# Performance work log

Measured on AMD Instinct MI355X. Metric: run time of the kernel, lower is better.

## Reference

```python
import jax, jax.numpy as jnp
import numpy as np

KEEP_RATIO = 0.1
FS = 8          # feature_size
BN_EPS = 1e-5


def dct_matrix(N):
    # Orthonormal DCT-II matrix: D[k,n] = s_k * cos(pi*(2n+1)*k/(2N))
    n = jnp.arange(N, dtype=jnp.float32)
    k = n[:, None]
    D = jnp.cos(jnp.pi * (2.0 * n + 1.0) * k / (2.0 * N))
    scale = jnp.full((N, 1), jnp.sqrt(2.0 / N), jnp.float32).at[0, 0].set(jnp.sqrt(1.0 / N))
    return D * scale


def bilinear_resize(x, out_h, out_w):
    # torch F.interpolate bilinear, align_corners=False (half-pixel centers, no antialias)
    def coords(in_size, out):
        src = (jnp.arange(out, dtype=jnp.float32) + 0.5) * (in_size / out) - 0.5
        src = jnp.clip(src, 0.0, in_size - 1.0)
        i0 = jnp.floor(src).astype(jnp.int32)
        i1 = jnp.minimum(i0 + 1, in_size - 1)
        return i0, i1, src - i0.astype(jnp.float32)
    r0, r1, rw = coords(x.shape[2], out_h)
    c0, c1, cw = coords(x.shape[3], out_w)
    x = x[:, :, r0, :] * (1.0 - rw)[:, None] + x[:, :, r1, :] * rw[:, None]
    x = x[:, :, :, c0] * (1.0 - cw) + x[:, :, :, c1] * cw
    return x


def apply_dct(x):
    H, W = x.shape[2], x.shape[3]
    Dh, Dw = dct_matrix(H), dct_matrix(W)
    # 2D DCT-II (ortho): Y = Dh @ X @ Dw^T
    y = jnp.einsum('hi,bcij,wj->bchw', Dh, x, Dw)
    hk, wk = int(H * KEEP_RATIO), int(W * KEEP_RATIO)
    mask = jnp.zeros((H, W), x.dtype).at[:hk, :wk].set(1.0)  # low-pass keep top-left block
    y = y * mask
    # inverse DCT (ortho): X = Dh^T @ Y @ Dw
    x = jnp.einsum('ih,bchw,jw->bcij', Dh, y, Dw)
    return bilinear_resize(x, FS, FS)


def generate_gradient_image(x):
    # scipy convolve2d flips the kernel, but flipped sobel == -sobel and we take abs,
    # so plain correlation with sobel is equivalent. boundary='wrap' -> circular pad.
    sx = jnp.array([[-1, 0, 1], [-2, 0, 2], [-1, 0, 1]], jnp.float32)
    sy = jnp.array([[-1, -2, -1], [0, 0, 0], [1, 2, 1]], jnp.float32)
    kern = jnp.stack([sx, sy])[:, None]  # [2,1,3,3]
    B, C, H, W = x.shape
    xc = x.reshape(B * C, 1, H, W)
    xp = jnp.pad(xc, ((0, 0), (0, 0), (1, 1), (1, 1)), mode='wrap')
    g = jax.lax.conv_general_dilated(xp, kern, (1, 1), 'VALID')  # [B*C,2,H,W]
    grad = jnp.sqrt(g[:, 0] ** 2 + g[:, 1] ** 2).reshape(B, C, H, W)
    return bilinear_resize(grad, FS, FS)


def feature_extractor(x, w, b, gamma, beta):
    y = jax.lax.conv_general_dilated(x, w, (1, 1), ((1, 1), (1, 1)))
    y = y + b[None, :, None, None]
    # BatchNorm (inference: running_mean=0, running_var=1)
    y = y * (gamma / jnp.sqrt(1.0 + BN_EPS))[None, :, None, None] + beta[None, :, None, None]
    y = jax.nn.relu(y)
    # input is already FS x FS, so AdaptiveAvgPool2d((8,8)) is the identity
    return y


def setup_inputs() -> dict:
    key = jax.random.key(0)
    ks = jax.random.split(key, 10)
    B, C, H, W = 128, 3, 256, 256
    return {
        'x': jax.random.normal(ks[0], (B, C, H, W), jnp.float32),
        'conv_dct_w': jax.random.normal(ks[1], (64, 3, 3, 3), jnp.float32) * 0.1,
        'conv_dct_b': jnp.zeros((64,), jnp.float32),
        'bn_dct_g': jnp.ones((64,), jnp.float32),
        'bn_dct_b': jnp.zeros((64,), jnp.float32),
        'conv_grad_w': jax.random.normal(ks[2], (64, 3, 3, 3), jnp.float32) * 0.1,
        'conv_grad_b': jnp.zeros((64,), jnp.float32),
        'bn_grad_g': jnp.ones((64,), jnp.float32),
        'bn_grad_b': jnp.zeros((64,), jnp.float32),
        'fus_w': jax.random.normal(ks[3], (1, 64), jnp.float32) * 0.1,
        'fus_b': jnp.zeros((1,), jnp.float32),
        'cls_w': jax.random.normal(ks[4], (2, 64 * FS * FS), jnp.float32) * 0.02,
        'cls_b': jnp.zeros((2,), jnp.float32),
    }


def reference(x, conv_dct_w, conv_dct_b, bn_dct_g, bn_dct_b,
              conv_grad_w, conv_grad_b, bn_grad_g, bn_grad_b,
              fus_w, fus_b, cls_w, cls_b):
    dct_in = apply_dct(x)                       # [B,3,8,8]
    grad_in = generate_gradient_image(x)        # [B,3,8,8]
    d = feature_extractor(dct_in, conv_dct_w, conv_dct_b, bn_dct_g, bn_dct_b)    # [B,64,8,8]
    g = feature_extractor(grad_in, conv_grad_w, conv_grad_b, bn_grad_g, bn_grad_b)
    # FeatureFusion: weight = sigmoid(fc(avgpool(d+g)))
    s = jnp.mean(d + g, axis=(2, 3))            # [B,64]
    w = jax.nn.sigmoid(s @ fus_w.T + fus_b)     # [B,1]
    w = w[:, :, None, None]
    fused = w * d + (1.0 - w) * g               # [B,64,8,8]
    flat = fused.reshape(fused.shape[0], -1)
    return flat @ cls_w.T + cls_b               # [B,2]
```

## Files before the change

kernel.cpp:

```cpp
#include <hip/hip_runtime.h>
#include <math.h>


__global__ __launch_bounds__(256) void k_compute_Et(float* __restrict__ Et) {
    __shared__ float F[8][25];
    const int tid = threadIdx.x;
    const float pi_f = 3.14159274101257324f;
    if (tid < 25) {
        const int k = tid;
        const float scale = (k == 0) ? sqrtf(1.0f / 256.0f) : sqrtf(2.0f / 256.0f);
        for (int p = 0; p < 8; ++p) {
            const int n0 = 32 * p + 15;
            const float a0 = (pi_f * (float)(2 * n0 + 1)) * (float)k / 512.0f;
            const float a1 = (pi_f * (float)(2 * n0 + 3)) * (float)k / 512.0f;
            F[p][k] = 0.5f * (cosf(a0) + cosf(a1)) * scale;
        }
    }
    __syncthreads();
    const int j = tid;
    float acc[8] = {0.f, 0.f, 0.f, 0.f, 0.f, 0.f, 0.f, 0.f};
    for (int k = 0; k < 25; ++k) {
        const float scale = (k == 0) ? sqrtf(1.0f / 256.0f) : sqrtf(2.0f / 256.0f);
        const float arg = (pi_f * (float)(2 * j + 1)) * (float)k / 512.0f;
        const float Dkj = cosf(arg) * scale;
        #pragma unroll
        for (int p = 0; p < 8; ++p) acc[p] = fmaf(F[p][k], Dkj, acc[p]);
    }
    #pragma unroll
    for (int p = 0; p < 8; ++p) Et[j * 8 + p] = acc[p];
}

__global__ __launch_bounds__(512) void k_dct(const float* __restrict__ x,
                                             const float* __restrict__ Etg,
                                             float* __restrict__ dct_out) {
    __shared__ float Et[256][8];
    __shared__ float T[8][256];
    __shared__ float PO[8][64];

    const int img = blockIdx.x;
    const float* xi = x + (size_t)img * 65536;
    const int tid = threadIdx.x;

    float* etf = &Et[0][0];
    for (int i = tid; i < 2048; i += 512) etf[i] = Etg[i];
    __syncthreads();

    const int w = tid >> 6, l = tid & 63;
    const int cw = w >> 1, ch = w & 1;
    const int col = ch * 128 + 2 * l;

    float acc[8][2];
    #pragma unroll
    for (int p = 0; p < 8; ++p) { acc[p][0] = 0.f; acc[p][1] = 0.f; }

    const float* px = xi + (size_t)(cw * 64) * 256 + col;
    #pragma unroll 4
    for (int i = 0; i < 64; ++i) {
        const float2 v = *(const float2*)px;
        px += 256;
        const int row = cw * 64 + i;
        const float4 ea = *(const float4*)&Et[row][0];
        const float4 eb = *(const float4*)&Et[row][4];
        acc[0][0] = fmaf(ea.x, v.x, acc[0][0]); acc[0][1] = fmaf(ea.x, v.y, acc[0][1]);
        acc[1][0] = fmaf(ea.y, v.x, acc[1][0]); acc[1][1] = fmaf(ea.y, v.y, acc[1][1]);
        acc[2][0] = fmaf(ea.z, v.x, acc[2][0]); acc[2][1] = fmaf(ea.z, v.y, acc[2][1]);
        acc[3][0] = fmaf(ea.w, v.x, acc[3][0]); acc[3][1] = fmaf(ea.w, v.y, acc[3][1]);
        acc[4][0] = fmaf(eb.x, v.x, acc[4][0]); acc[4][1] = fmaf(eb.x, v.y, acc[4][1]);
        acc[5][0] = fmaf(eb.y, v.x, acc[5][0]); acc[5][1] = fmaf(eb.y, v.y, acc[5][1]);
        acc[6][0] = fmaf(eb.z, v.x, acc[6][0]); acc[6][1] = fmaf(eb.z, v.y, acc[6][1]);
        acc[7][0] = fmaf(eb.w, v.x, acc[7][0]); acc[7][1] = fmaf(eb.w, v.y, acc[7][1]);
    }

    for (int r = 0; r < 4; ++r) {
        if (cw == r) {
            if (r == 0) {
                #pragma unroll
                for (int p = 0; p < 8; ++p) {
                    float2 t; t.x = acc[p][0]; t.y = acc[p][1];
                    *(float2*)&T[p][col] = t;
                }
            } else {
                #pragma unroll
                for (int p = 0; p < 8; ++p) {
                    float2 t = *(const float2*)&T[p][col];
                    t.x += acc[p][0]; t.y += acc[p][1];
                    *(float2*)&T[p][col] = t;
                }
            }
        }
        __syncthreads();
    }

    const int pq = tid & 63, seg = tid >> 6;
    const int p = pq >> 3, q = pq & 7;
    float s = 0.0f;
    const int j0 = seg * 32;
    for (int j = j0; j < j0 + 32; ++j) s = fmaf(T[p][j], Et[j][q], s);
    PO[seg][pq] = s;
    __syncthreads();
    if (tid < 64) {
        float r = PO[0][tid] + PO[1][tid] + PO[2][tid] + PO[3][tid] +
                  PO[4][tid] + PO[5][tid] + PO[6][tid] + PO[7][tid];
        dct_out[img * 64 + tid] = r;
    }
}

__global__ __launch_bounds__(256) void k_grad(const float* __restrict__ x,
                                              float* __restrict__ grad_out) {
    const int img = blockIdx.x;
    const int tid = threadIdx.x;
    const int s = tid & 3, pq = tid >> 2;
    const int p = pq >> 3, q = pq & 7;
    const int dr = s >> 1, dc = s & 1;
    const float* xi = x + (size_t)img * 65536;
    const int r = 32 * p + 15 + dr, c = 32 * q + 15 + dc;
    const float* base = xi + (r - 1) * 256 + (c - 1);
    const float a00 = base[0],   a01 = base[1],   a02 = base[2];
    const float a10 = base[256],                  a12 = base[258];
    const float a20 = base[512], a21 = base[513], a22 = base[514];
    const float gx = (a02 - a00) + 2.0f * (a12 - a10) + (a22 - a20);
    const float gy = (a20 - a00) + 2.0f * (a21 - a01) + (a22 - a02);
    float m = sqrtf(gx * gx + gy * gy);
    m += __shfl_xor(m, 1);
    m += __shfl_xor(m, 2);
    if (s == 0) grad_out[img * 64 + pq] = 0.25f * m;
}

__global__ __launch_bounds__(256) void k_head(
    const float* __restrict__ dct_in, const float* __restrict__ grad_in,
    const float* __restrict__ wd, const float* __restrict__ bd,
    const float* __restrict__ gd, const float* __restrict__ betad,
    const float* __restrict__ wg, const float* __restrict__ bg,
    const float* __restrict__ gg, const float* __restrict__ betag,
    const float* __restrict__ fus_w, const float* __restrict__ fus_b,
    const float* __restrict__ cls_w, const float* __restrict__ cls_b,
    float* __restrict__ out) {
    __shared__ float ind[3][8][8];
    __shared__ float ing[3][8][8];
    __shared__ float wdl[1728];
    __shared__ float wgl[1728];
    __shared__ float redS[256];
    __shared__ float redF[64];
    __shared__ float redO0[256];
    __shared__ float redO1[256];
    __shared__ float wshare;

    const int b = blockIdx.x;
    const int tid = threadIdx.x;
    const int co = tid & 63;
    const int chunk = tid >> 6;

    float* pind = &ind[0][0][0];
    float* ping = &ing[0][0][0];
    for (int i = tid; i < 192; i += 256) {
        pind[i] = dct_in[b * 192 + i];
        ping[i] = grad_in[b * 192 + i];
    }
    for (int i = tid; i < 1728; i += 256) {
        wdl[i] = wd[i];
        wgl[i] = wg[i];
    }
    __syncthreads();

    const float scale_d = gd[co] / sqrtf(1.0f + 1e-5f);
    const float scale_g = gg[co] / sqrtf(1.0f + 1e-5f);
    const float beta_d = betad[co];
    const float beta_g = betag[co];
    const float bias_d = bd[co];
    const float bias_g = bg[co];

    float dreg[16], greg[16];
    float ssum = 0.0f;
    int idx = 0;
    for (int pr = chunk * 2; pr < chunk * 2 + 2; ++pr) {
        for (int qc = 0; qc < 8; ++qc) {
            float sd = bias_d, sg = bias_g;
            for (int ci = 0; ci < 3; ++ci) {
                #pragma unroll
                for (int du = 0; du < 3; ++du) {
                    const int r = pr + du - 1;
                    if (r < 0 || r > 7) continue;
                    #pragma unroll
                    for (int dv = 0; dv < 3; ++dv) {
                        const int c = qc + dv - 1;
                        if (c < 0 || c > 7) continue;
                        const float wv_d = wdl[co * 27 + ci * 9 + du * 3 + dv];
                        const float wv_g = wgl[co * 27 + ci * 9 + du * 3 + dv];
                        sd = fmaf(wv_d, ind[ci][r][c], sd);
                        sg = fmaf(wv_g, ing[ci][r][c], sg);
                    }
                }
            }
            sd = fmaxf(sd * scale_d + beta_d, 0.0f);
            sg = fmaxf(sg * scale_g + beta_g, 0.0f);
            dreg[idx] = sd;
            greg[idx] = sg;
            ssum += sd + sg;
            ++idx;
        }
    }

    redS[tid] = ssum;
    __syncthreads();
    if (tid < 64) {
        const float s =
            (redS[co] + redS[64 + co] + redS[128 + co] + redS[192 + co]) *
            (1.0f / 64.0f);
        redF[co] = s * fus_w[co];
    }
    __syncthreads();
    if (tid == 0) {
        float z = fus_b[0];
        for (int i = 0; i < 64; ++i) z += redF[i];
        wshare = 1.0f / (1.0f + expf(-z));
    }
    __syncthreads();
    const float wgt = wshare;

    float po0 = 0.0f, po1 = 0.0f;
    idx = 0;
    for (int pr = chunk * 2; pr < chunk * 2 + 2; ++pr) {
        for (int qc = 0; qc < 8; ++qc) {
            const float f = wgt * dreg[idx] + (1.0f - wgt) * greg[idx];
            const int n = co * 64 + pr * 8 + qc;
            po0 = fmaf(f, cls_w[n], po0);
            po1 = fmaf(f, cls_w[4096 + n], po1);
            ++idx;
        }
    }
    redO0[tid] = po0;
    redO1[tid] = po1;
    __syncthreads();
    if (tid < 64) {
        redO0[tid] += redO0[tid + 64] + redO0[tid + 128] + redO0[tid + 192];
        redO1[tid] += redO1[tid + 64] + redO1[tid + 128] + redO1[tid + 192];
    }
    __syncthreads();
    if (tid == 0) {
        float s = cls_b[0];
        for (int i = 0; i < 64; ++i) s += redO0[i];
        out[b * 2 + 0] = s;
    }
    if (tid == 1) {
        float s = cls_b[1];
        for (int i = 0; i < 64; ++i) s += redO1[i];
        out[b * 2 + 1] = s;
    }
}

extern "C" void kernel_launch(void* const* d_in, const int* in_sizes, int n_in,
                              void* d_out, int out_size, void* d_ws, size_t ws_size,
                              hipStream_t stream) {
    const float* x     = (const float*)d_in[0];
    const float* wd    = (const float*)d_in[1];
    const float* bd    = (const float*)d_in[2];
    const float* gd    = (const float*)d_in[3];
    const float* betad = (const float*)d_in[4];
    const float* wg    = (const float*)d_in[5];
    const float* bg    = (const float*)d_in[6];
    const float* gg    = (const float*)d_in[7];
    const float* betag = (const float*)d_in[8];
    const float* fusw  = (const float*)d_in[9];
    const float* fusb  = (const float*)d_in[10];
    const float* clsw  = (const float*)d_in[11];
    const float* clsb  = (const float*)d_in[12];
    float* out = (float*)d_out;

    float* ws = (float*)d_ws;
    float* Et      = ws;
    float* dct_in  = ws + 2048;
    float* grad_in = ws + 2048 + 24576;

    k_compute_Et<<<1, 256, 0, stream>>>(Et);
    k_grad<<<384, 256, 0, stream>>>(x, grad_in);
    k_dct<<<384, 512, 0, stream>>>(x, Et, dct_in);
    k_head<<<128, 256, 0, stream>>>(dct_in, grad_in, wd, bd, gd, betad,
                                    wg, bg, gg, betag, fusw, fusb, clsw, clsb,
                                    out);
}
```

Measured before the change: 197.0 us.

## Fuse Et computation, gradient and DCT into one kernel; restructure head classifier

Merges the Et-table kernel, the Sobel gradient kernel and the DCT kernel into a single launch. Each block now recomputes the Et projection table in shared memory, and the upper 256 threads compute the gradient samples. This removes two kernel launches and the global round-trip for Et, at the cost of redundant cosf work in every block. The head kernel also stages fused features in padded shared memory so cls_w reads are coalesced, and replaces serial reductions with wavefront shuffles.

```diff
diff --git a/kernel.cpp b/kernel.cpp
--- a/kernel.cpp
+++ b/kernel.cpp
@@ -2,11 +2,36 @@
 #include <math.h>
 
 
-__global__ __launch_bounds__(256) void k_compute_Et(float* __restrict__ Et) {
+__global__ __launch_bounds__(512) void k_main(const float* __restrict__ x,
+                                              float* __restrict__ dct_out,
+                                              float* __restrict__ grad_out) {
     __shared__ float F[8][25];
+    __shared__ float Et[256][8];
+    __shared__ float T[8][256];
+    __shared__ float PO[8][64];
+
+    const int img = blockIdx.x;
+    const float* xi = x + (size_t)img * 65536;
     const int tid = threadIdx.x;
     const float pi_f = 3.14159274101257324f;
-    if (tid < 25) {
+
+    if (tid >= 256) {
+        const int t = tid - 256;
+        const int s = t & 3, pq = t >> 2;
+        const int p = pq >> 3, q = pq & 7;
+        const int dr = s >> 1, dc = s & 1;
+        const int r = 32 * p + 15 + dr, c = 32 * q + 15 + dc;
+        const float* base = xi + (r - 1) * 256 + (c - 1);
+        const float a00 = base[0],   a01 = base[1],   a02 = base[2];
+        const float a10 = base[256],                  a12 = base[258];
+        const float a20 = base[512], a21 = base[513], a22 = base[514];
+        const float gx = (a02 - a00) + 2.0f * (a12 - a10) + (a22 - a20);
+        const float gy = (a20 - a00) + 2.0f * (a21 - a01) + (a22 - a02);
+        float m = sqrtf(gx * gx + gy * gy);
+        m += __shfl_xor(m, 1);
+        m += __shfl_xor(m, 2);
+        if (s == 0) grad_out[img * 64 + pq] = 0.25f * m;
+    } else if (tid < 25) {
         const int k = tid;
         const float scale = (k == 0) ? sqrtf(1.0f / 256.0f) : sqrtf(2.0f / 256.0f);
         for (int p = 0; p < 8; ++p) {
@@ -17,32 +42,20 @@
         }
     }
     __syncthreads();
-    const int j = tid;
-    float acc[8] = {0.f, 0.f, 0.f, 0.f, 0.f, 0.f, 0.f, 0.f};
-    for (int k = 0; k < 25; ++k) {
-        const float scale = (k == 0) ? sqrtf(1.0f / 256.0f) : sqrtf(2.0f / 256.0f);
-        const float arg = (pi_f * (float)(2 * j + 1)) * (float)k / 512.0f;
-        const float Dkj = cosf(arg) * scale;
+
+    if (tid < 256) {
+        const int j = tid;
+        float acc[8] = {0.f, 0.f, 0.f, 0.f, 0.f, 0.f, 0.f, 0.f};
+        for (int k = 0; k < 25; ++k) {
+            const float scale = (k == 0) ? sqrtf(1.0f / 256.0f) : sqrtf(2.0f / 256.0f);
+            const float arg = (pi_f * (float)(2 * j + 1)) * (float)k / 512.0f;
+            const float Dkj = cosf(arg) * scale;
+            #pragma unroll
+            for (int p = 0; p < 8; ++p) acc[p] = fmaf(F[p][k], Dkj, acc[p]);
+        }
         #pragma unroll
-        for (int p = 0; p < 8; ++p) acc[p] = fmaf(F[p][k], Dkj, acc[p]);
-    }
-    #pragma unroll
-    for (int p = 0; p < 8; ++p) Et[j * 8 + p] = acc[p];
-}
-
-__global__ __launch_bounds__(512) void k_dct(const float* __restrict__ x,
-                                             const float* __restrict__ Etg,
-                                             float* __restrict__ dct_out) {
-    __shared__ float Et[256][8];
-    __shared__ float T[8][256];
-    __shared__ float PO[8][64];
-
-    const int img = blockIdx.x;
-    const float* xi = x + (size_t)img * 65536;
-    const int tid = threadIdx.x;
-
-    float* etf = &Et[0][0];
-    for (int i = tid; i < 2048; i += 512) etf[i] = Etg[i];
+        for (int p = 0; p < 8; ++p) Et[j][p] = acc[p];
+    }
     __syncthreads();
 
     const int w = tid >> 6, l = tid & 63;
@@ -105,27 +118,6 @@
     }
 }
 
-__global__ __launch_bounds__(256) void k_grad(const float* __restrict__ x,
-                                              float* __restrict__ grad_out) {
-    const int img = blockIdx.x;
-    const int tid = threadIdx.x;
-    const int s = tid & 3, pq = tid >> 2;
-    const int p = pq >> 3, q = pq & 7;
-    const int dr = s >> 1, dc = s & 1;
-    const float* xi = x + (size_t)img * 65536;
-    const int r = 32 * p + 15 + dr, c = 32 * q + 15 + dc;
-    const float* base = xi + (r - 1) * 256 + (c - 1);
-    const float a00 = base[0],   a01 = base[1],   a02 = base[2];
-    const float a10 = base[256],                  a12 = base[258];
-    const float a20 = base[512], a21 = base[513], a22 = base[514];
-    const float gx = (a02 - a00) + 2.0f * (a12 - a10) + (a22 - a20);
-    const float gy = (a20 - a00) + 2.0f * (a21 - a01) + (a22 - a02);
-    float m = sqrtf(gx * gx + gy * gy);
-    m += __shfl_xor(m, 1);
-    m += __shfl_xor(m, 2);
-    if (s == 0) grad_out[img * 64 + pq] = 0.25f * m;
-}
-
 __global__ __launch_bounds__(256) void k_head(
     const float* __restrict__ dct_in, const float* __restrict__ grad_in,
     const float* __restrict__ wd, const float* __restrict__ bd,
@@ -141,8 +133,9 @@
     __shared__ float wgl[1728];
     __shared__ float redS[256];
     __shared__ float redF[64];
-    __shared__ float redO0[256];
-    __shared__ float redO1[256];
+    __shared__ float fusedS[64][65];
+    __shared__ float redW0[4];
+    __shared__ float redW1[4];
     __shared__ float wshare;
 
     const int b = blockIdx.x;
@@ -209,43 +202,43 @@
         redF[co] = s * fus_w[co];
     }
     __syncthreads();
-    if (tid == 0) {
-        float z = fus_b[0];
-        for (int i = 0; i < 64; ++i) z += redF[i];
-        wshare = 1.0f / (1.0f + expf(-z));
+    if (tid < 64) {
+        float v = redF[tid];
+        #pragma unroll
+        for (int off = 1; off < 64; off <<= 1) v += __shfl_xor(v, off);
+        if (tid == 0) wshare = 1.0f / (1.0f + expf(-(v + fus_b[0])));
     }
     __syncthreads();
     const float wgt = wshare;
 
-    float po0 = 0.0f, po1 = 0.0f;
     idx = 0;
     for (int pr = chunk * 2; pr < chunk * 2 + 2; ++pr) {
         for (int qc = 0; qc < 8; ++qc) {
             const float f = wgt * dreg[idx] + (1.0f - wgt) * greg[idx];
-            const int n = co * 64 + pr * 8 + qc;
-            po0 = fmaf(f, cls_w[n], po0);
-            po1 = fmaf(f, cls_w[4096 + n], po1);
+            fusedS[co][pr * 8 + qc] = f;
             ++idx;
         }
     }
-    redO0[tid] = po0;
-    redO1[tid] = po1;
-    __syncthreads();
-    if (tid < 64) {
-        redO0[tid] += redO0[tid + 64] + redO0[tid + 128] + redO0[tid + 192];
-        redO1[tid] += redO1[tid + 64] + redO1[tid + 128] + redO1[tid + 192];
-    }
-    __syncthreads();
-    if (tid == 0) {
-        float s = cls_b[0];
-        for (int i = 0; i < 64; ++i) s += redO0[i];
-        out[b * 2 + 0] = s;
-    }
-    if (tid == 1) {
-        float s = cls_b[1];
-        for (int i = 0; i < 64; ++i) s += redO1[i];
-        out[b * 2 + 1] = s;
-    }
+    __syncthreads();
+
+    const int l = tid & 63, wv = tid >> 6;
+    float a0 = 0.0f, a1 = 0.0f;
+    #pragma unroll
+    for (int k = 0; k < 16; ++k) {
+        const int n = tid + 256 * k;
+        const float f = fusedS[wv + 4 * k][l];
+        a0 = fmaf(f, cls_w[n], a0);
+        a1 = fmaf(f, cls_w[4096 + n], a1);
+    }
+    #pragma unroll
+    for (int off = 1; off < 64; off <<= 1) {
+        a0 += __shfl_xor(a0, off);
+        a1 += __shfl_xor(a1, off);
+    }
+    if (l == 0) { redW0[wv] = a0; redW1[wv] = a1; }
+    __syncthreads();
+    if (tid == 0) out[b * 2 + 0] = cls_b[0] + redW0[0] + redW0[1] + redW0[2] + redW0[3];
+    if (tid == 1) out[b * 2 + 1] = cls_b[1] + redW1[0] + redW1[1] + redW1[2] + redW1[3];
 }
 
 extern "C" void kernel_launch(void* const* d_in, const int* in_sizes, int n_in,
@@ -267,13 +260,10 @@
     float* out = (float*)d_out;
 
     float* ws = (float*)d_ws;
-    float* Et      = ws;
-    float* dct_in  = ws + 2048;
-    float* grad_in = ws + 2048 + 24576;
-
-    k_compute_Et<<<1, 256, 0, stream>>>(Et);
-    k_grad<<<384, 256, 0, stream>>>(x, grad_in);
-    k_dct<<<384, 512, 0, stream>>>(x, Et, dct_in);
+    float* dct_in  = ws;
+    float* grad_in = ws + 24576;
+
+    k_main<<<384, 512, 0, stream>>>(x, dct_in, grad_in);
     k_head<<<128, 256, 0, stream>>>(dct_in, grad_in, wd, bd, gd, betad,
                                     wg, bg, gg, betag, fusw, fusb, clsw, clsb,
                                     out);
```

After: 189.3 us. -3.9%, faster.
